# Performance work log

Hardware: AMD Instinct MI355X
Metric: run time of the kernel (lower is better)

## Reference

```python
import jax, jax.numpy as jnp
import numpy as np

B, H, S, D = 2, 16, 2048, 128
BLOCK_N = 64          # key-block size used by the Triton inner loop (BLOCK_N<=HEAD_DIM configs)
CAUSAL = True
NEG = -1000000.0      # kernel masks with -1e6, not -inf
LOG2E = 1.44269504


def _round_away(x):
    # tl.math.floor(|x| + 0.5) * sign(x): round half away from zero
    return jnp.floor(jnp.abs(x) + 0.5) * jnp.where(x >= 0, 1.0, -1.0)


def _quant_per_token(x):
    # per-(B,H,S) symmetric int8 quantization (values kept in fp32; exact, since |q|<=127)
    amax = jnp.maximum(jnp.max(jnp.abs(x), axis=-1), 1e-8)
    scale = amax / 127.0
    xq = jnp.clip(_round_away(x / scale[..., None]), -127.0, 127.0)
    return xq, scale


def _quant_per_head(v):
    # per-(B,H) symmetric int8 quantization
    amax = jnp.maximum(jnp.max(jnp.abs(v), axis=(-2, -1)), 1e-8)
    scale = amax / 127.0
    vq = jnp.clip(_round_away(v / scale[..., None, None]), -127.0, 127.0)
    return vq, scale


def _forward(q, k, v, sm_scale):
    q_q, q_s = _quant_per_token(q)   # [B,H,S,D], [B,H,S]
    k_q, k_s = _quant_per_token(k)
    v_q, v_s = _quant_per_head(v)    # [B,H,S,D], [B,H]

    nb = S // BLOCK_N
    k_blk = k_q.reshape(B, H, nb, BLOCK_N, D).transpose(2, 0, 1, 3, 4)   # [nb,B,H,Bn,D]
    ks_blk = k_s.reshape(B, H, nb, BLOCK_N).transpose(2, 0, 1, 3)        # [nb,B,H,Bn]
    v_blk = v_q.reshape(B, H, nb, BLOCK_N, D).transpose(2, 0, 1, 3, 4)   # [nb,B,H,Bn,D]
    cols = jnp.arange(S, dtype=jnp.int32).reshape(nb, BLOCK_N)
    rows = jnp.arange(S, dtype=jnp.int32)

    qk_scale = sm_scale * LOG2E
    vs_term = v_s[:, :, None, None] / 127.0  # [B,H,1,1]

    def step(carry, xs):
        m, l, acc = carry
        kb, ksb, vb, cb = xs
        # int8 QK^T dequantized: exact in fp32 (|sum| <= 127*127*128 < 2^24)
        qk = jnp.einsum('bhsd,bhnd->bhsn', q_q, kb)
        qk = qk * q_s[..., None] * ksb[:, :, None, :] * qk_scale
        if CAUSAL:
            qk = jnp.where(rows[:, None] >= cb[None, :], qk, NEG)
        m_new = jnp.maximum(m, jnp.max(qk, axis=-1))
        p = jnp.exp2(qk - m_new[..., None])
        # online quantization of probabilities at block-local running max (as in kernel)
        p_q = jnp.floor(p * 127.0 + 0.5)
        alpha = jnp.exp2(m - m_new)
        l = l * alpha + jnp.sum(p, axis=-1)
        acc = acc * alpha[..., None] + jnp.einsum('bhsn,bhnd->bhsd', p_q, vb) * vs_term
        return (m_new, l, acc), None

    m0 = jnp.full((B, H, S), -jnp.inf, dtype=jnp.float32)
    l0 = jnp.ones((B, H, S), dtype=jnp.float32)   # killed by alpha=exp2(-inf)=0 at first block
    acc0 = jnp.zeros((B, H, S, D), dtype=jnp.float32)
    (m, l, acc), _ = jax.lax.scan(jax.checkpoint(step), (m0, l0, acc0),
                                  (k_blk, ks_blk, v_blk, cols))
    return acc / l[..., None]


def setup_inputs() -> dict:
    key = jax.random.key(0)
    kq, kk, kv = jax.random.split(key, 3)
    q = jax.random.normal(kq, (B, H, S, D), dtype=jnp.float32)
    k = jax.random.normal(kk, (B, H, S, D), dtype=jnp.float32)
    v = jax.random.normal(kv, (B, H, S, D), dtype=jnp.float32)
    sm_scale = jnp.float32(1.0 / np.sqrt(D))
    return {"q": q, "k": k, "v": v, "sm_scale": sm_scale}


def reference(q, k, v, sm_scale):
    return _forward(q, k, v, sm_scale)
```

## Files before the change

kernel.cpp:

```cpp
#include <hip/hip_runtime.h>

#define S_LEN 2048
#define D_DIM 128
#define NBH   32
#define LOG2E 1.44269504f
#define NEGM  -1000000.0f

typedef __bf16 bf16x8 __attribute__((ext_vector_type(8)));
typedef short  s16x8  __attribute__((ext_vector_type(8)));
typedef float  f32x4  __attribute__((ext_vector_type(4)));
typedef float  f32x16 __attribute__((ext_vector_type(16)));
typedef unsigned int u32x4 __attribute__((ext_vector_type(4)));

static __device__ __forceinline__ unsigned short f32_to_bf16_bits_exact(float f) {
    return (unsigned short)(__float_as_uint(f) >> 16);
}
static __device__ __forceinline__ float round_away(float t) {
    float r = floorf(fabsf(t) + 0.5f);
    return (t >= 0.0f) ? r : -r;
}
static __device__ __forceinline__ unsigned int pq_pack(float p0, float p1) {
    float a = floorf(fmaf(p0, 127.0f, 0.5f));
    float b = floorf(fmaf(p1, 127.0f, 0.5f));
    return __builtin_amdgcn_perm(__float_as_uint(b), __float_as_uint(a), 0x07060302);
}

__global__ __launch_bounds__(256) void quant_qkv_kernel(
    const float* __restrict__ q, const float* __restrict__ k,
    const float* __restrict__ v,
    unsigned short* __restrict__ qq, unsigned short* __restrict__ kq,
    float* __restrict__ qs, float* __restrict__ ks,
    unsigned int* __restrict__ vab)
{
    if (blockIdx.x < 16384) {
        const int R = NBH * S_LEN;
        int w   = blockIdx.x * 8 + (threadIdx.x >> 5);
        int l32 = threadIdx.x & 31;
        const float* src; unsigned short* dq; float* ds; int row;
        if (w < R) { src = q; dq = qq; ds = qs; row = w; }
        else       { src = k; dq = kq; ds = ks; row = w - R; }
        size_t base = (size_t)row * D_DIM + l32 * 4;
        float4 x = *(const float4*)(src + base);
        float amax = fmaxf(fmaxf(fabsf(x.x), fabsf(x.y)), fmaxf(fabsf(x.z), fabsf(x.w)));
        #pragma unroll
        for (int m = 1; m < 32; m <<= 1) amax = fmaxf(amax, __shfl_xor(amax, m));
        float scale = fmaxf(amax, 1e-8f) / 127.0f;
        ushort4 o;
        o.x = f32_to_bf16_bits_exact(fminf(fmaxf(round_away(x.x / scale), -127.0f), 127.0f));
        o.y = f32_to_bf16_bits_exact(fminf(fmaxf(round_away(x.y / scale), -127.0f), 127.0f));
        o.z = f32_to_bf16_bits_exact(fminf(fmaxf(round_away(x.z / scale), -127.0f), 127.0f));
        o.w = f32_to_bf16_bits_exact(fminf(fmaxf(round_away(x.w / scale), -127.0f), 127.0f));
        *(ushort4*)(dq + base) = o;
        if (l32 == 0) ds[row] = scale;
    } else {
        int bid2 = blockIdx.x - 16384;
        int bh = bid2 >> 3, blk = bid2 & 7;
        const float4* base = (const float4*)(v + (size_t)bh * S_LEN * D_DIM) + blk * 8192;
        int t = threadIdx.x;
        float am = 0.0f;
        #pragma unroll
        for (int i = 0; i < 32; ++i) {
            float4 x = base[t + i * 256];
            am = fmaxf(am, fmaxf(fmaxf(fabsf(x.x), fabsf(x.y)), fmaxf(fabsf(x.z), fabsf(x.w))));
        }
        #pragma unroll
        for (int m = 1; m < 64; m <<= 1) am = fmaxf(am, __shfl_xor(am, m));
        __shared__ float red[4];
        if ((t & 63) == 0) red[t >> 6] = am;
        __syncthreads();
        if (t == 0) {
            float a = fmaxf(fmaxf(red[0], red[1]), fmaxf(red[2], red[3]));
            atomicMax(&vab[bh], __float_as_uint(a));
        }
    }
}

__global__ __launch_bounds__(256) void vtq_kernel(const float* __restrict__ v,
                                                  const unsigned int* __restrict__ vab,
                                                  unsigned short* __restrict__ vT)
{
    __shared__ unsigned short tileT[128][72];
    int bh = blockIdx.x >> 5, sb = blockIdx.x & 31;
    float scale = fmaxf(__uint_as_float(vab[bh]), 1e-8f) / 127.0f;
    int t = threadIdx.x;
    const float* src = v + ((size_t)bh * S_LEN + sb * 64) * D_DIM;
    #pragma unroll
    for (int it = 0; it < 8; ++it) {
        int c = t + it * 256;
        int rs = c >> 5, c4 = (c & 31) * 4;
        float4 x = *(const float4*)(src + rs * D_DIM + c4);
        float vals[4] = {x.x, x.y, x.z, x.w};
        #pragma unroll
        for (int u = 0; u < 4; ++u) {
            float r = fminf(fmaxf(round_away(vals[u] / scale), -127.0f), 127.0f);
            tileT[c4 + u][rs] = f32_to_bf16_bits_exact(r);
        }
    }
    __syncthreads();
    unsigned short* dst = vT + (size_t)bh * D_DIM * S_LEN + sb * 64;
    #pragma unroll
    for (int it = 0; it < 4; ++it) {
        int c = t + it * 256;
        int d = c >> 3, c8 = (c & 7) * 8;
        *(s16x8*)(dst + (size_t)d * S_LEN + c8) = *(const s16x8*)&tileT[d][c8];
    }
}

__global__ __launch_bounds__(512, 2) void attn_kernel(
    const unsigned short* __restrict__ qq,
    const unsigned short* __restrict__ kq,
    const unsigned short* __restrict__ vT,
    const float* __restrict__ qs,
    const float* __restrict__ ks,
    const unsigned int* __restrict__ vab,
    const float* __restrict__ smp,
    float* __restrict__ out)
{
    extern __shared__ char smem[];

    const int tid  = threadIdx.x;
    const int lane = tid & 63;
    const int wid  = tid >> 6;
    const int w4   = wid & 3;
    const int half = wid >> 2;
    const int c32  = lane & 31;
    const int hi   = lane >> 5;
    const int t8   = tid & 255;

    char*   KbH  = smem + half * 16384;
    char*   VbH  = smem + 32768 + half * 16384;
    float*  ksl  = (float*)(smem + 65536);
    float2* ML   = (float2*)(smem + 73728);
    char*   Qlds = smem + 75776;
    float*  Ol   = (float*)smem;

    const int bid = blockIdx.x;
    const int qb  = 15 - (bid >> 5);
    const int bh  = bid & 31;

    const float qk_scale = smp[0] * LOG2E;
    const float vscale   = fmaxf(__uint_as_float(vab[bh]), 1e-8f) / 127.0f;
    const float vs_term  = vscale / 127.0f;

    const int   q  = qb * 128 + c32 * 4 + w4;
    const float qf = qs[(size_t)bh * S_LEN + q] * qk_scale;

    const char* kqb = (const char*)(kq + (size_t)bh * S_LEN * D_DIM);
    const char* vtb = (const char*)(vT + (size_t)bh * D_DIM * S_LEN);

    ((f32x4*)ksl)[tid] = ((const f32x4*)(ks + (size_t)bh * S_LEN))[tid];
    {
        const char* qqb = (const char*)(qq + ((size_t)bh * S_LEN + qb * 128) * D_DIM);
        #pragma unroll
        for (int it = 0; it < 4; ++it) {
            int L = (tid + it * 512) * 16;
            int w = L >> 13, Lw = L & 8191;
            int r = Lw >> 8, x = Lw & 255;
            int col = x ^ ((r & 15) << 4);
            *(s16x8*)(Qlds + L) = *(const s16x8*)(qqb + (r * 4 + w) * 256 + col);
        }
    }

    int kOff[4], vOff[4], lOff[4];
    #pragma unroll
    for (int it = 0; it < 4; ++it) {
        int L = (t8 + it * 256) * 16;
        lOff[it] = L;
        int r = L >> 8, x = L & 255;
        int c = x ^ ((r & 15) << 4);
        kOff[it] = (half * 64 + r) * 256 + c;
        int rho = L >> 9, xv = L & 511;
        int cv  = xv ^ ((rho & 15) << 4);
        vOff[it] = ((cv >> 7) * 32 + rho) * (S_LEN * 2) + half * 128 + (cv & 127);
    }

    float mrow = -100.0f;
    float lrow = 0.0f;
    f32x16 oacc0, oacc1, oacc2, oacc3;
    #pragma unroll
    for (int i = 0; i < 16; ++i) { oacc0[i] = 0.f; oacc1[i] = 0.f; oacc2[i] = 0.f; oacc3[i] = 0.f; }

    const int swz = (c32 & 15) << 4;
    const char* aBase = KbH + c32 * 256;
    const char* bBase = Qlds + w4 * 8192 + c32 * 256;
    const char* vBase = VbH + c32 * 512;

    const int jn_d = qb + 1;

    s16x8 kpre[4], vpre[4];
    #pragma unroll
    for (int it = 0; it < 4; ++it) {
        kpre[it] = *(const s16x8*)(kqb + kOff[it]);
        vpre[it] = *(const s16x8*)(vtb + vOff[it]);
    }

    auto iter = [&](const int d, const bool domask) __attribute__((always_inline)) {
        __syncthreads();
        #pragma unroll
        for (int it = 0; it < 4; ++it) *(s16x8*)(KbH + lOff[it]) = kpre[it];
        #pragma unroll
        for (int it = 0; it < 4; ++it) *(s16x8*)(VbH + lOff[it]) = vpre[it];
        if (d + 1 < jn_d) {
            const int jb2 = (d + 1) * 128;
            #pragma unroll
            for (int it = 0; it < 4; ++it) {
                kpre[it] = *(const s16x8*)(kqb + jb2 * 256 + kOff[it]);
                vpre[it] = *(const s16x8*)(vtb + jb2 * 2   + vOff[it]);
            }
        }
        __syncthreads();

        f32x16 sc0, sc1;
        #pragma unroll
        for (int i = 0; i < 16; ++i) { sc0[i] = 0.f; sc1[i] = 0.f; }
        #pragma unroll
        for (int st = 0; st < 8; ++st) {
            int cB = (st * 32 + hi * 16) ^ swz;
            bf16x8 a0 = __builtin_bit_cast(bf16x8, *(const s16x8*)(aBase + cB));
            bf16x8 a1 = __builtin_bit_cast(bf16x8, *(const s16x8*)(aBase + 32 * 256 + cB));
            bf16x8 b  = __builtin_bit_cast(bf16x8, *(const s16x8*)(bBase + cB));
            sc0 = __builtin_amdgcn_mfma_f32_32x32x16_bf16(a0, b, sc0, 0, 0, 0);
            sc1 = __builtin_amdgcn_mfma_f32_32x32x16_bf16(a1, b, sc1, 0, 0, 0);
        }

        const int jbh = d * 128 + half * 64;
        float mhA = -3.0e38f, mhB = -3.0e38f;
        #pragma unroll
        for (int gg = 0; gg < 4; ++gg) {
            f32x4 kv0 = *(const f32x4*)&ksl[jbh + gg * 8 + hi * 4];
            f32x4 kv1 = *(const f32x4*)&ksl[jbh + 32 + gg * 8 + hi * 4];
            #pragma unroll
            for (int i = 0; i < 4; ++i) {
                int r = gg * 4 + i;
                float tv0 = fmaf(sc0[r], qf * kv0[i], -mrow);
                float tv1 = fmaf(sc1[r], qf * kv1[i], -mrow);
                if (domask) {
                    int key0 = jbh + gg * 8 + i + hi * 4;
                    tv0 = (q >= key0)      ? tv0 : NEGM;
                    tv1 = (q >= key0 + 32) ? tv1 : NEGM;
                }
                sc0[r] = tv0; sc1[r] = tv1;
                if (i & 1) mhB = fmaxf(mhB, fmaxf(tv0, tv1));
                else       mhA = fmaxf(mhA, fmaxf(tv0, tv1));
            }
        }
        float mh     = fmaxf(mhA, mhB);
        float vmax_t = fmaxf(mh, __shfl_xor(mh, 32));

        if (__any(vmax_t > 1.0f)) {
            float sh    = fmaxf(vmax_t, 0.0f);
            float alpha = exp2f(-sh);
            mrow += sh;
            #pragma unroll
            for (int r = 0; r < 16; ++r) { sc0[r] -= sh; sc1[r] -= sh; }
            oacc0 *= alpha; oacc1 *= alpha; oacc2 *= alpha; oacc3 *= alpha;
            lrow  *= alpha;
        }

        float ts[8];
        #pragma unroll
        for (int r = 0; r < 8; ++r) {
            sc0[r]     = exp2f(sc0[r]);
            sc0[r + 8] = exp2f(sc0[r + 8]);
            sc1[r]     = exp2f(sc1[r]);
            sc1[r + 8] = exp2f(sc1[r + 8]);
            ts[r] = (sc0[r] + sc0[r + 8]) + (sc1[r] + sc1[r + 8]);
        }
        #pragma unroll
        for (int stp = 4; stp >= 1; stp >>= 1)
            #pragma unroll
            for (int r = 0; r < stp; ++r) ts[r] += ts[r + stp];
        lrow += ts[0] + __shfl_xor(ts[0], 32);

        unsigned int W0[8], W1[8];
        #pragma unroll
        for (int gg = 0; gg < 4; ++gg) {
            W0[gg*2+0] = pq_pack(sc0[gg*4+0], sc0[gg*4+1]);
            W0[gg*2+1] = pq_pack(sc0[gg*4+2], sc0[gg*4+3]);
            W1[gg*2+0] = pq_pack(sc1[gg*4+0], sc1[gg*4+1]);
            W1[gg*2+1] = pq_pack(sc1[gg*4+2], sc1[gg*4+3]);
        }
        #pragma unroll
        for (int s = 0; s < 2; ++s) {
            asm("v_permlane32_swap_b32 %0, %1" : "+v"(W0[s*4+0]), "+v"(W0[s*4+2]));
            asm("v_permlane32_swap_b32 %0, %1" : "+v"(W0[s*4+1]), "+v"(W0[s*4+3]));
            asm("v_permlane32_swap_b32 %0, %1" : "+v"(W1[s*4+0]), "+v"(W1[s*4+2]));
            asm("v_permlane32_swap_b32 %0, %1" : "+v"(W1[s*4+1]), "+v"(W1[s*4+3]));
        }
        #pragma unroll
        for (int t = 0; t < 2; ++t) {
            const unsigned int* Wt = t ? W1 : W0;
            #pragma unroll
            for (int s = 0; s < 2; ++s) {
                u32x4 uw; uw.x = Wt[s*4+0]; uw.y = Wt[s*4+1]; uw.z = Wt[s*4+2]; uw.w = Wt[s*4+3];
                bf16x8 bfrag = __builtin_bit_cast(bf16x8, uw);
                int cb = t * 64 + s * 32 + hi * 16;
                bf16x8 va;
                va = __builtin_bit_cast(bf16x8, *(const s16x8*)(vBase + ((cb +   0) ^ swz)));
                oacc0 = __builtin_amdgcn_mfma_f32_32x32x16_bf16(va, bfrag, oacc0, 0, 0, 0);
                va = __builtin_bit_cast(bf16x8, *(const s16x8*)(vBase + ((cb + 128) ^ swz)));
                oacc1 = __builtin_amdgcn_mfma_f32_32x32x16_bf16(va, bfrag, oacc1, 0, 0, 0);
                va = __builtin_bit_cast(bf16x8, *(const s16x8*)(vBase + ((cb + 256) ^ swz)));
                oacc2 = __builtin_amdgcn_mfma_f32_32x32x16_bf16(va, bfrag, oacc2, 0, 0, 0);
                va = __builtin_bit_cast(bf16x8, *(const s16x8*)(vBase + ((cb + 384) ^ swz)));
                oacc3 = __builtin_amdgcn_mfma_f32_32x32x16_bf16(va, bfrag, oacc3, 0, 0, 0);
            }
        }
    };

    for (int d = 0; d < jn_d - 1; ++d) iter(d, false);
    iter(jn_d - 1, true);

    __syncthreads();
    if (hi == 0) { float2 ml2; ml2.x = mrow; ml2.y = lrow; ML[half * 128 + w4 * 32 + c32] = ml2; }
    __syncthreads();
    float2 mo  = ML[(1 - half) * 128 + w4 * 32 + c32];
    float  mfin = fmaxf(mrow, mo.x);
    float  bs  = exp2f(mrow - mfin);
    float  bo  = exp2f(mo.x - mfin);
    float  lfin = lrow * bs + mo.y * bo;
    const float inv = bs * vs_term / lfin;

    for (int pass = 0; pass < 2; ++pass) {
        __syncthreads();
        if (half == 0 && (w4 >> 1) == pass) {
            float* reg = Ol + (w4 & 1) * 4224 + c32 * 132;
            #pragma unroll
            for (int r = 0; r < 16; ++r) {
                int drow = (r & 3) + 8 * (r >> 2) + 4 * hi;
                reg[drow]      = oacc0[r] * inv;
                reg[drow + 32] = oacc1[r] * inv;
                reg[drow + 64] = oacc2[r] * inv;
                reg[drow + 96] = oacc3[r] * inv;
            }
        }
        __syncthreads();
        if (half == 1 && (w4 >> 1) == pass) {
            float* reg = Ol + (w4 & 1) * 4224 + c32 * 132;
            #pragma unroll
            for (int r = 0; r < 16; ++r) {
                int drow = (r & 3) + 8 * (r >> 2) + 4 * hi;
                reg[drow]      += oacc0[r] * inv;
                reg[drow + 32] += oacc1[r] * inv;
                reg[drow + 64] += oacc2[r] * inv;
                reg[drow + 96] += oacc3[r] * inv;
            }
        }
        __syncthreads();
        #pragma unroll
        for (int it = 0; it < 4; ++it) {
            int idx = tid + it * 512;
            int w2  = idx >> 10;
            int rem = idx & 1023;
            int row = rem >> 5, c4 = rem & 31;
            f32x4 v4 = *(const f32x4*)(Ol + w2 * 4224 + row * 132 + c4 * 4);
            int qr = qb * 128 + row * 4 + pass * 2 + w2;
            *(f32x4*)(out + ((size_t)bh * S_LEN + qr) * D_DIM + c4 * 4) = v4;
        }
    }
}

extern "C" void kernel_launch(void* const* d_in, const int* in_sizes, int n_in,
                              void* d_out, int out_size, void* d_ws, size_t ws_size,
                              hipStream_t stream)
{
    const float* q  = (const float*)d_in[0];
    const float* k  = (const float*)d_in[1];
    const float* v  = (const float*)d_in[2];
    const float* sm = (const float*)d_in[3];

    if (ws_size < (size_t)50857000) return;
    char* ws = (char*)d_ws;
    unsigned short* qq = (unsigned short*)(ws);
    unsigned short* kq = (unsigned short*)(ws + (1u << 24));
    unsigned short* vT = (unsigned short*)(ws + (2u << 24));
    float*          qs = (float*)(ws + (3u << 24));
    float*          ks = (float*)(ws + (3u << 24) + 262144);
    unsigned int*  vab = (unsigned int*)(ws + (3u << 24) + 524288);
    float*         out = (float*)d_out;

    hipFuncSetAttribute((const void*)attn_kernel,
                        hipFuncAttributeMaxDynamicSharedMemorySize, 108544);

    hipMemsetAsync(vab, 0, NBH * sizeof(unsigned int), stream);
    quant_qkv_kernel<<<dim3(16640), dim3(256), 0, stream>>>(q, k, v, qq, kq, qs, ks, vab);
    vtq_kernel<<<dim3(1024), dim3(256), 0, stream>>>(v, vab, vT);
    attn_kernel<<<dim3(512), dim3(512), 108544, stream>>>(qq, kq, vT, qs, ks, vab, sm, out);
}
```

Baseline: 111.1 us.

## Double-buffer K/V tiles in LDS and hold Q fragments in registers

```diff
diff --git a/kernel.cpp b/kernel.cpp
--- a/kernel.cpp
+++ b/kernel.cpp
@@ -127,11 +127,8 @@
     const int hi   = lane >> 5;
     const int t8   = tid & 255;
 
-    char*   KbH  = smem + half * 16384;
-    char*   VbH  = smem + 32768 + half * 16384;
-    float*  ksl  = (float*)(smem + 65536);
-    float2* ML   = (float2*)(smem + 73728);
-    char*   Qlds = smem + 75776;
+    float*  ksl  = (float*)(smem + 131072);
+    float2* ML   = (float2*)(smem + 139264);
     float*  Ol   = (float*)smem;
 
     const int bid = blockIdx.x;
@@ -149,16 +146,12 @@
     const char* vtb = (const char*)(vT + (size_t)bh * D_DIM * S_LEN);
 
     ((f32x4*)ksl)[tid] = ((const f32x4*)(ks + (size_t)bh * S_LEN))[tid];
+    bf16x8 qfrag[8];
     {
-        const char* qqb = (const char*)(qq + ((size_t)bh * S_LEN + qb * 128) * D_DIM);
-        #pragma unroll
-        for (int it = 0; it < 4; ++it) {
-            int L = (tid + it * 512) * 16;
-            int w = L >> 13, Lw = L & 8191;
-            int r = Lw >> 8, x = Lw & 255;
-            int col = x ^ ((r & 15) << 4);
-            *(s16x8*)(Qlds + L) = *(const s16x8*)(qqb + (r * 4 + w) * 256 + col);
-        }
+        const char* qrow = (const char*)(qq + ((size_t)bh * S_LEN + q) * D_DIM);
+        #pragma unroll
+        for (int st = 0; st < 8; ++st)
+            qfrag[st] = __builtin_bit_cast(bf16x8, *(const s16x8*)(qrow + st * 32 + hi * 16));
     }
 
     int kOff[4], vOff[4], lOff[4];
@@ -181,10 +174,6 @@
     for (int i = 0; i < 16; ++i) { oacc0[i] = 0.f; oacc1[i] = 0.f; oacc2[i] = 0.f; oacc3[i] = 0.f; }
 
     const int swz = (c32 & 15) << 4;
-    const char* aBase = KbH + c32 * 256;
-    const char* bBase = Qlds + w4 * 8192 + c32 * 256;
-    const char* vBase = VbH + c32 * 512;
-
     const int jn_d = qb + 1;
 
     s16x8 kpre[4], vpre[4];
@@ -194,21 +183,26 @@
         vpre[it] = *(const s16x8*)(vtb + vOff[it]);
     }
 
-    auto iter = [&](const int d, const bool domask) __attribute__((always_inline)) {
-        __syncthreads();
-        #pragma unroll
-        for (int it = 0; it < 4; ++it) *(s16x8*)(KbH + lOff[it]) = kpre[it];
-        #pragma unroll
-        for (int it = 0; it < 4; ++it) *(s16x8*)(VbH + lOff[it]) = vpre[it];
-        if (d + 1 < jn_d) {
-            const int jb2 = (d + 1) * 128;
+    {
+        char* Kd = smem + half * 16384;
+        char* Vd = smem + 65536 + half * 16384;
+        #pragma unroll
+        for (int it = 0; it < 4; ++it) *(s16x8*)(Kd + lOff[it]) = kpre[it];
+        #pragma unroll
+        for (int it = 0; it < 4; ++it) *(s16x8*)(Vd + lOff[it]) = vpre[it];
+        if (jn_d > 1) {
             #pragma unroll
             for (int it = 0; it < 4; ++it) {
-                kpre[it] = *(const s16x8*)(kqb + jb2 * 256 + kOff[it]);
-                vpre[it] = *(const s16x8*)(vtb + jb2 * 2   + vOff[it]);
-            }
-        }
-        __syncthreads();
+                kpre[it] = *(const s16x8*)(kqb + 128 * 256 + kOff[it]);
+                vpre[it] = *(const s16x8*)(vtb + 128 * 2   + vOff[it]);
+            }
+        }
+    }
+    __syncthreads();
+
+    auto compute = [&](const int d, const bool domask) __attribute__((always_inline)) {
+        const char* aBase = smem + (d & 1) * 32768 + half * 16384 + c32 * 256;
+        const char* vB    = smem + 65536 + (d & 1) * 32768 + half * 16384 + c32 * 512;
 
         f32x16 sc0, sc1;
         #pragma unroll
@@ -218,9 +212,8 @@
             int cB = (st * 32 + hi * 16) ^ swz;
             bf16x8 a0 = __builtin_bit_cast(bf16x8, *(const s16x8*)(aBase + cB));
             bf16x8 a1 = __builtin_bit_cast(bf16x8, *(const s16x8*)(aBase + 32 * 256 + cB));
-            bf16x8 b  = __builtin_bit_cast(bf16x8, *(const s16x8*)(bBase + cB));
-            sc0 = __builtin_amdgcn_mfma_f32_32x32x16_bf16(a0, b, sc0, 0, 0, 0);
-            sc1 = __builtin_amdgcn_mfma_f32_32x32x16_bf16(a1, b, sc1, 0, 0, 0);
+            sc0 = __builtin_amdgcn_mfma_f32_32x32x16_bf16(a0, qfrag[st], sc0, 0, 0, 0);
+            sc1 = __builtin_amdgcn_mfma_f32_32x32x16_bf16(a1, qfrag[st], sc1, 0, 0, 0);
         }
 
         const int jbh = d * 128 + half * 64;
@@ -296,20 +289,37 @@
                 bf16x8 bfrag = __builtin_bit_cast(bf16x8, uw);
                 int cb = t * 64 + s * 32 + hi * 16;
                 bf16x8 va;
-                va = __builtin_bit_cast(bf16x8, *(const s16x8*)(vBase + ((cb +   0) ^ swz)));
+                va = __builtin_bit_cast(bf16x8, *(const s16x8*)(vB + ((cb +   0) ^ swz)));
                 oacc0 = __builtin_amdgcn_mfma_f32_32x32x16_bf16(va, bfrag, oacc0, 0, 0, 0);
-                va = __builtin_bit_cast(bf16x8, *(const s16x8*)(vBase + ((cb + 128) ^ swz)));
+                va = __builtin_bit_cast(bf16x8, *(const s16x8*)(vB + ((cb + 128) ^ swz)));
                 oacc1 = __builtin_amdgcn_mfma_f32_32x32x16_bf16(va, bfrag, oacc1, 0, 0, 0);
-                va = __builtin_bit_cast(bf16x8, *(const s16x8*)(vBase + ((cb + 256) ^ swz)));
+                va = __builtin_bit_cast(bf16x8, *(const s16x8*)(vB + ((cb + 256) ^ swz)));
                 oacc2 = __builtin_amdgcn_mfma_f32_32x32x16_bf16(va, bfrag, oacc2, 0, 0, 0);
-                va = __builtin_bit_cast(bf16x8, *(const s16x8*)(vBase + ((cb + 384) ^ swz)));
+                va = __builtin_bit_cast(bf16x8, *(const s16x8*)(vB + ((cb + 384) ^ swz)));
                 oacc3 = __builtin_amdgcn_mfma_f32_32x32x16_bf16(va, bfrag, oacc3, 0, 0, 0);
             }
         }
     };
 
-    for (int d = 0; d < jn_d - 1; ++d) iter(d, false);
-    iter(jn_d - 1, true);
+    for (int d = 0; d < jn_d - 1; ++d) {
+        char* Kd = smem + ((d + 1) & 1) * 32768 + half * 16384;
+        char* Vd = smem + 65536 + ((d + 1) & 1) * 32768 + half * 16384;
+        #pragma unroll
+        for (int it = 0; it < 4; ++it) *(s16x8*)(Kd + lOff[it]) = kpre[it];
+        #pragma unroll
+        for (int it = 0; it < 4; ++it) *(s16x8*)(Vd + lOff[it]) = vpre[it];
+        if (d + 2 < jn_d) {
+            const int jb2 = (d + 2) * 128;
+            #pragma unroll
+            for (int it = 0; it < 4; ++it) {
+                kpre[it] = *(const s16x8*)(kqb + jb2 * 256 + kOff[it]);
+                vpre[it] = *(const s16x8*)(vtb + jb2 * 2   + vOff[it]);
+            }
+        }
+        compute(d, false);
+        __syncthreads();
+    }
+    compute(jn_d - 1, true);
 
     __syncthreads();
     if (hi == 0) { float2 ml2; ml2.x = mrow; ml2.y = lrow; ML[half * 128 + w4 * 32 + c32] = ml2; }
@@ -380,10 +390,10 @@
     float*         out = (float*)d_out;
 
     hipFuncSetAttribute((const void*)attn_kernel,
-                        hipFuncAttributeMaxDynamicSharedMemorySize, 108544);
+                        hipFuncAttributeMaxDynamicSharedMemorySize, 141312);
 
     hipMemsetAsync(vab, 0, NBH * sizeof(unsigned int), stream);
     quant_qkv_kernel<<<dim3(16640), dim3(256), 0, stream>>>(q, k, v, qq, kq, qs, ks, vab);
     vtq_kernel<<<dim3(1024), dim3(256), 0, stream>>>(v, vab, vT);
-    attn_kernel<<<dim3(512), dim3(512), 108544, stream>>>(qq, kq, vT, qs, ks, vab, sm, out);
-}
+    attn_kernel<<<dim3(512), dim3(512), 141312, stream>>>(qq, kq, vT, qs, ks, vab, sm, out);
+}
```

After: 112.1 us. No clear change (+0.9%).
